# Kernel optimization log

Hardware: AMD Instinct MI355X
Metric: run time of the kernel (lower is better)

## Reference

```python
import jax, jax.numpy as jnp
import numpy as np

N = 512          # nodes per sample (num_nodes)
B = 8            # batch size (samples)
H = 64           # hidden_dim
SPARSITY = 0.1
K = int(SPARSITY * N * (N - 1))  # edges kept per sample (fixed, static)


def setup_inputs() -> dict:
    key = jax.random.key(0)
    ks = jax.random.split(key, 8)

    def lin(k, fi, fo):
        w = jax.random.normal(k, (fi, fo), jnp.float32) / np.sqrt(fi).astype(np.float32)
        b = jnp.zeros((fo,), jnp.float32)
        return w, b

    w_emb, b_emb = lin(ks[0], 1, H)
    w_proj, b_proj = lin(ks[1], H, H)
    w1, b1 = lin(ks[2], 2 * H, H)
    w2, b2 = lin(ks[3], H, H // 2)
    w3, b3 = lin(ks[4], H // 2, 1)
    x = jax.random.uniform(ks[5], (B * N, 1), jnp.float32)  # abundances >= 0
    batch = jnp.repeat(jnp.arange(B, dtype=jnp.int32), N)   # [B*N]
    return dict(x=x, w_emb=w_emb, b_emb=b_emb, w_proj=w_proj, b_proj=b_proj,
                w1=w1, b1=b1, w2=w2, b2=b2, w3=w3, b3=b3, batch=batch)


def reference(x, w_emb, b_emb, w_proj, b_proj, w1, b1, w2, b2, w3, b3, batch):
    # node embedding + projection (dropout is eval-mode no-op)
    emb = jax.nn.relu(x @ w_emb + b_emb) @ w_proj + b_proj     # [B*N, H]
    emb = emb.reshape(B, N, H)
    # first pairwise-MLP layer: cat([e_i, e_j]) @ w1 == e_i @ w1a + e_j @ w1b
    w1a, w1b = w1[:H], w1[H:]
    ai = emb @ w1a                                            # [B, N, H]
    aj = emb @ w1b                                            # [B, N, H]
    h1 = jax.nn.relu(ai[:, :, None, :] + aj[:, None, :, :] + b1)   # [B, N, N, H]
    h2 = jax.nn.relu(jnp.einsum('bijh,hk->bijk', h1, w2) + b2)     # [B, N, N, H/2]
    probs = jax.nn.sigmoid(jnp.einsum('bijk,ko->bij', h2, w3) + b3[0])  # [B, N, N]
    probs = 0.5 * (probs + jnp.swapaxes(probs, 1, 2))          # symmetrize
    probs = probs * (1.0 - jnp.eye(N, dtype=probs.dtype))      # mask diagonal
    flat = probs.reshape(B, N * N)
    _, idx = jax.lax.top_k(flat, K)                            # [B, K]
    idx = jnp.sort(idx, axis=-1)                               # row-major order (dense_to_sparse)
    vals = jnp.take_along_axis(flat, idx, axis=-1)             # [B, K]
    offsets = (jnp.arange(B) * N)[:, None]                     # node offset per sample
    rows = idx // N + offsets
    cols = idx % N + offsets
    edge_index = jnp.stack([rows.reshape(-1), cols.reshape(-1)], axis=0)  # [2, B*K]
    edge_weights = vals.reshape(-1)                            # [B*K]
    adj = jnp.zeros((B, N * N), flat.dtype).at[jnp.arange(B)[:, None], idx].set(vals)
    adj = adj.reshape(B, N, N)                                 # sparse adjacency per sample
    return edge_index, edge_weights, adj
```

## Files before the change

kernel.cpp:

```cpp
#include <hip/hip_runtime.h>

#define NV 512
#define BV 8
#define KSEL 26163
#define NNv (NV*NV)
#define BKv (BV*KSEL)
#define CAPB 32768
#define DELTA 1e-4f

typedef unsigned int u32;
typedef __attribute__((ext_vector_type(2))) float f32x2;
typedef __attribute__((ext_vector_type(4))) float f32x4;
typedef __attribute__((ext_vector_type(4))) u32 u32x4;
typedef __attribute__((ext_vector_type(8))) _Float16 f16x8;

__device__ __forceinline__ f32x2 pk_add(f32x2 a, f32x2 b) {
    f32x2 d; asm("v_pk_add_f32 %0, %1, %2" : "=v"(d) : "v"(a), "v"(b)); return d;
}
__device__ __forceinline__ f32x2 pk_mul(f32x2 a, f32x2 b) {
    f32x2 d; asm("v_pk_mul_f32 %0, %1, %2" : "=v"(d) : "v"(a), "v"(b)); return d;
}
__device__ __forceinline__ f32x2 pk_fma(f32x2 a, f32x2 b, f32x2 c) {
    f32x2 d; asm("v_pk_fma_f32 %0, %1, %2, %3" : "=v"(d) : "v"(a), "v"(b), "v"(c)); return d;
}
__device__ __forceinline__ u32 pkrtz(float a, float b) {
    u32 d; asm("v_cvt_pkrtz_f16_f32 %0, %1, %2" : "=v"(d) : "v"(a), "v"(b)); return d;
}

__global__ void __launch_bounds__(256) k_embed(
    const float* __restrict__ x, const float* __restrict__ w_emb,
    const float* __restrict__ b_emb, const float* __restrict__ w_proj,
    const float* __restrict__ b_proj, const float* __restrict__ w1,
    const float* __restrict__ b1,
    float* __restrict__ ai, float* __restrict__ aj,
    float* __restrict__ ai256, float* __restrict__ ajb256) {
    __shared__ float sh[4][64];
    __shared__ float se[4][64];
    const int c = threadIdx.x;
    const int lr = threadIdx.y;
    const int row = blockIdx.x * 4 + lr;
    const float xv = x[row];
    sh[lr][c] = fmaxf(fmaf(xv, w_emb[c], b_emb[c]), 0.f);
    __syncthreads();
    float e = 0.f;
#pragma unroll
    for (int h = 0; h < 64; ++h) e = fmaf(sh[lr][h], w_proj[h * 64 + c], e);
    se[lr][c] = e + b_proj[c];
    __syncthreads();
    float a0 = 0.f, a1 = 0.f;
#pragma unroll
    for (int h = 0; h < 64; ++h) {
        const float ev = se[lr][h];
        a0 = fmaf(ev, w1[h * 64 + c], a0);
        a1 = fmaf(ev, w1[(64 + h) * 64 + c], a1);
    }
    ai[row * 64 + c] = a0;
    aj[row * 64 + c] = a1;
    ai256[row * 64 + c] = a0 * 256.0f;
    ajb256[row * 64 + c] = (a1 + b1[c]) * 256.0f;
}

__global__ void __launch_bounds__(256) k_pairs_sym(
    const float* __restrict__ ai256, const float* __restrict__ ajb256,
    const float* __restrict__ w2, const float* __restrict__ b2,
    const float* __restrict__ w3, const float* __restrict__ b3,
    float* __restrict__ probs, u32* __restrict__ hist8) {
    __shared__ float sI[2048];
    __shared__ float sJ[2048];
    __shared__ float sp1[32 * 36];
    __shared__ float sp2[32 * 36];
    __shared__ u32 lh[1024];
    const int tid = threadIdx.x;
    const int b = blockIdx.y;
    int remb = blockIdx.x, ta = 0;
    while (remb >= 16 - ta) { remb -= 16 - ta; ++ta; }
    const int tb = ta + remb;
    const int i0 = ta << 5, j0 = tb << 5;
    {
        const int r = tid >> 3, c8 = (tid & 7) << 3;
        const float* srcI = &ai256[(((b << 9) + i0 + r) << 6) + c8];
        *(float4*)&sI[(r << 6) + c8]     = *(const float4*)&srcI[0];
        *(float4*)&sI[(r << 6) + c8 + 4] = *(const float4*)&srcI[4];
        const float* srcJ = &ai256[(((b << 9) + j0 + r) << 6) + c8];
        *(float4*)&sJ[(r << 6) + c8]     = *(const float4*)&srcJ[0];
        *(float4*)&sJ[(r << 6) + c8 + 4] = *(const float4*)&srcJ[4];
        lh[tid] = 0; lh[256 + tid] = 0; lh[512 + tid] = 0; lh[768 + tid] = 0;
    }
    const int lane = tid & 63;
    const int lp = lane & 15, lg = lane >> 4;
    const int wave = tid >> 6;
    const int dir = wave >> 1, wc = wave & 1;
    const int colb = (wc << 4) + lp;
    const int colg = (dir ? i0 : j0) + colb;

    alignas(16) float ajr[2][8];
    {
        const float* base = &ajb256[(((b << 9) + colg) << 6) + (lg << 3)];
        *(float4*)&ajr[0][0] = *(const float4*)&base[0];
        *(float4*)&ajr[0][4] = *(const float4*)&base[4];
        *(float4*)&ajr[1][0] = *(const float4*)&base[32];
        *(float4*)&ajr[1][4] = *(const float4*)&base[36];
    }
    f16x8 Ah[2][2], Al[2][2];
#pragma unroll
    for (int kt = 0; kt < 2; ++kt)
#pragma unroll
        for (int ch = 0; ch < 2; ++ch)
#pragma unroll
            for (int e = 0; e < 8; ++e) {
                const float wv2 = w2[((ch << 5) + (lg << 3) + e) * 32 + (kt << 4) + lp];
                const _Float16 wh = (_Float16)wv2;
                Ah[kt][ch][e] = wh;
                Al[kt][ch][e] = (_Float16)((wv2 - (float)wh) * 2048.0f);
            }
    float b2f[2][4], w3f[2][4];
#pragma unroll
    for (int kt = 0; kt < 2; ++kt)
#pragma unroll
        for (int r = 0; r < 4; ++r) {
            b2f[kt][r] = b2[(kt << 4) + (lg << 2) + r] * 256.0f;
            w3f[kt][r] = w3[(kt << 4) + (lg << 2) + r] * 0.00390625f;
        }
    const float b3v = b3[0];
    __syncthreads();

    const float* __restrict__ sA = dir ? sJ : sI;
    float* __restrict__ spO = dir ? sp2 : sp1;
    const f32x2 C2048 = {2048.f, 2048.f};
    const f32x2 CN2048 = {-2048.f, -2048.f};

    for (int r = 0; r < 32; ++r) {
        alignas(16) float ar[2][8];
        *(float4*)&ar[0][0] = *(const float4*)&sA[(r << 6) + (lg << 3)];
        *(float4*)&ar[0][4] = *(const float4*)&sA[(r << 6) + (lg << 3) + 4];
        *(float4*)&ar[1][0] = *(const float4*)&sA[(r << 6) + 32 + (lg << 3)];
        *(float4*)&ar[1][4] = *(const float4*)&sA[(r << 6) + 32 + (lg << 3) + 4];
        alignas(16) u32 hw[2][4], lw[2][4];
#pragma unroll
        for (int c = 0; c < 2; ++c)
#pragma unroll
            for (int e2 = 0; e2 < 4; ++e2) {
                const f32x2 a2 = *(const f32x2*)&ar[c][e2 * 2];
                const f32x2 j2 = *(const f32x2*)&ajr[c][e2 * 2];
                const f32x2 t2 = pk_add(a2, j2);
                const float u0 = fmaxf(t2[0], 0.f);
                const float u1 = fmaxf(t2[1], 0.f);
                hw[c][e2] = pkrtz(u0, u1);
                f32x2 u2; u2[0] = u0; u2[1] = u1;
                f32x2 hif;
                hif[0] = __uint_as_float(__float_as_uint(u0) & 0xFFFFE000u);
                hif[1] = __uint_as_float(__float_as_uint(u1) & 0xFFFFE000u);
                const f32x2 tm = pk_mul(u2, C2048);
                const f32x2 lo = pk_fma(hif, CN2048, tm);
                lw[c][e2] = pkrtz(lo[0], lo[1]);
            }
        const f16x8 Bh0 = __builtin_bit_cast(f16x8, *(u32x4*)&hw[0][0]);
        const f16x8 Bh1 = __builtin_bit_cast(f16x8, *(u32x4*)&hw[1][0]);
        const f16x8 Bl0 = __builtin_bit_cast(f16x8, *(u32x4*)&lw[0][0]);
        const f16x8 Bl1 = __builtin_bit_cast(f16x8, *(u32x4*)&lw[1][0]);
        f32x4 am0 = {0.f,0.f,0.f,0.f}, am1 = {0.f,0.f,0.f,0.f};
        f32x4 ac0 = {0.f,0.f,0.f,0.f}, ac1 = {0.f,0.f,0.f,0.f};
        am0 = __builtin_amdgcn_mfma_f32_16x16x32_f16(Ah[0][0], Bh0, am0, 0, 0, 0);
        am0 = __builtin_amdgcn_mfma_f32_16x16x32_f16(Ah[0][1], Bh1, am0, 0, 0, 0);
        ac0 = __builtin_amdgcn_mfma_f32_16x16x32_f16(Ah[0][0], Bl0, ac0, 0, 0, 0);
        ac0 = __builtin_amdgcn_mfma_f32_16x16x32_f16(Ah[0][1], Bl1, ac0, 0, 0, 0);
        ac0 = __builtin_amdgcn_mfma_f32_16x16x32_f16(Al[0][0], Bh0, ac0, 0, 0, 0);
        ac0 = __builtin_amdgcn_mfma_f32_16x16x32_f16(Al[0][1], Bh1, ac0, 0, 0, 0);
        am1 = __builtin_amdgcn_mfma_f32_16x16x32_f16(Ah[1][0], Bh0, am1, 0, 0, 0);
        am1 = __builtin_amdgcn_mfma_f32_16x16x32_f16(Ah[1][1], Bh1, am1, 0, 0, 0);
        ac1 = __builtin_amdgcn_mfma_f32_16x16x32_f16(Ah[1][0], Bl0, ac1, 0, 0, 0);
        ac1 = __builtin_amdgcn_mfma_f32_16x16x32_f16(Ah[1][1], Bl1, ac1, 0, 0, 0);
        ac1 = __builtin_amdgcn_mfma_f32_16x16x32_f16(Al[1][0], Bh0, ac1, 0, 0, 0);
        ac1 = __builtin_amdgcn_mfma_f32_16x16x32_f16(Al[1][1], Bh1, ac1, 0, 0, 0);
        float s = 0.f;
#pragma unroll
        for (int q = 0; q < 4; ++q) {
            const float amc = fmaf(ac0[q], 4.8828125e-4f, am0[q]);
            s = fmaf(fmaxf(amc + b2f[0][q], 0.f), w3f[0][q], s);
        }
#pragma unroll
        for (int q = 0; q < 4; ++q) {
            const float amc = fmaf(ac1[q], 4.8828125e-4f, am1[q]);
            s = fmaf(fmaxf(amc + b2f[1][q], 0.f), w3f[1][q], s);
        }
        s += __shfl_xor(s, 16);
        s += __shfl_xor(s, 32);
        const float p = 1.f / (1.f + __expf(-(s + b3v)));
        if (lane < 16) {
            if (dir == 0) spO[r * 36 + colb] = p;
            else          spO[colb * 36 + r] = p;
        }
    }
    __syncthreads();

    {
        const int pr = tid >> 3;
        const int pc = (tid & 7) << 2;
        const int rep = (tid & 3) << 8;
        const bool diag = (ta == tb);
        float4 vo;
        float vq[4];
#pragma unroll
        for (int q = 0; q < 4; ++q) {
            float v = 0.5f * (sp1[pr * 36 + pc + q] + sp2[pr * 36 + pc + q]);
            if (diag && pr == pc + q) v = 0.f;
            vq[q] = v;
            atomicAdd(&lh[rep + (__float_as_uint(v) >> 24)], diag ? 1u : 2u);
        }
        vo.x = vq[0]; vo.y = vq[1]; vo.z = vq[2]; vo.w = vq[3];
        *(float4*)&probs[(((b << 9) + i0 + pr) << 9) + j0 + pc] = vo;
        if (!diag) {
            const int qr = tid >> 3;
            const int qc = (tid & 7) << 2;
            float4 w4;
            w4.x = 0.5f * (sp1[(qc + 0) * 36 + qr] + sp2[(qc + 0) * 36 + qr]);
            w4.y = 0.5f * (sp1[(qc + 1) * 36 + qr] + sp2[(qc + 1) * 36 + qr]);
            w4.z = 0.5f * (sp1[(qc + 2) * 36 + qr] + sp2[(qc + 2) * 36 + qr]);
            w4.w = 0.5f * (sp1[(qc + 3) * 36 + qr] + sp2[(qc + 3) * 36 + qr]);
            *(float4*)&probs[(((b << 9) + j0 + qr) << 9) + i0 + qc] = w4;
        }
    }
    __syncthreads();
    const u32 sum = lh[tid] + lh[256 + tid] + lh[512 + tid] + lh[768 + tid];
    if (sum) atomicAdd(&hist8[b * 256 + tid], sum);
}

__global__ void k_selp8(const u32* __restrict__ hist8, u32* __restrict__ c8,
                        u32* __restrict__ rem1) {
    __shared__ u32 s[256];
    const int b = blockIdx.x, t = threadIdx.x;
    s[t] = hist8[b * 256 + t];
    __syncthreads();
    for (int off = 1; off < 256; off <<= 1) {
        const u32 v = (t + off < 256) ? s[t + off] : 0u;
        __syncthreads();
        s[t] += v;
        __syncthreads();
    }
    const u32 above = (t < 255) ? s[t + 1] : 0u;
    if (s[t] >= (u32)KSEL && above < (u32)KSEL) {
        c8[b] = (u32)t;
        rem1[b] = (u32)KSEL - above;
    }
}

__global__ void __launch_bounds__(256) k_hist13(
    const float* __restrict__ probs, const u32* __restrict__ c8,
    u32* __restrict__ hist13) {
    __shared__ u32 lh[8192];
    const int t = threadIdx.x;
    for (int k = t; k < 8192; k += 256) lh[k] = 0u;
    __syncthreads();
    const int b = blockIdx.y;
    const u32 sel = c8[b];
    const float* Pb = probs + b * NNv;
    const int base = blockIdx.x * 4096 + t;
#pragma unroll
    for (int e = 0; e < 16; ++e) {
        const u32 key = __float_as_uint(Pb[base + e * 256]);
        if ((key >> 24) == sel) atomicAdd(&lh[(key >> 11) & 8191u], 1u);
    }
    __syncthreads();
    for (int k = t; k < 8192; k += 256) {
        const u32 v = lh[k];
        if (v) atomicAdd(&hist13[b * 8192 + k], v);
    }
}

__global__ void k_sel13(const u32* __restrict__ hist13, const u32* __restrict__ c8,
                        const u32* __restrict__ rem1, float* __restrict__ thr) {
    __shared__ u32 s[256];
    const int b = blockIdx.x, t = threadIdx.x;
    const u32* H = hist13 + b * 8192;
    u32 sum = 0;
    for (int k = 0; k < 32; ++k) sum += H[t * 32 + k];
    s[t] = sum;
    __syncthreads();
    for (int off = 1; off < 256; off <<= 1) {
        const u32 v = (t + off < 256) ? s[t + off] : 0u;
        __syncthreads();
        s[t] += v;
        __syncthreads();
    }
    const u32 remv = rem1[b];
    const u32 above = (t < 255) ? s[t + 1] : 0u;
    if (s[t] >= remv && above < remv) {
        u32 cum = above;
        int c = 31;
        for (; c >= 0; --c) {
            cum += H[t * 32 + c];
            if (cum >= remv) break;
        }
        const u32 p21 = (c8[b] << 13) | (u32)(t * 32 + c);
        thr[b]     = __uint_as_float(p21 << 11) - 2.f * DELTA;
        thr[8 + b] = __uint_as_float((p21 + 1u) << 11) + 2.f * DELTA;
    }
}

__global__ void __launch_bounds__(256) k_band(
    const float* __restrict__ P, const float* __restrict__ thr,
    u32* __restrict__ C_in, u32* __restrict__ bandCnt, u32* __restrict__ bandIdx,
    u32* __restrict__ bgt) {
    __shared__ u32 lidx[2048];
    __shared__ u32 lcnt, lhi, gbase;
    const int b = blockIdx.y, blk = blockIdx.x, t = threadIdx.x;
    if (t == 0) { lcnt = 0u; lhi = 0u; }
    __syncthreads();
    const float Tlo = thr[b], Thi = thr[8 + b];
    const int fi0 = blk * 1024 + t * 4;
    const float4 v = *(const float4*)&P[b * NNv + fi0];
    const float vv[4] = {v.x, v.y, v.z, v.w};
    u32 hc = 0;
#pragma unroll
    for (int q = 0; q < 4; ++q) {
        const float xq = vv[q];
        if (xq > Thi) ++hc;
        else if (xq >= Tlo) {
            const u32 p = atomicAdd(&lcnt, 1u);
            if (p < 2048u) lidx[p] = (u32)(fi0 + q);
        }
    }
    if (hc) atomicAdd(&lhi, hc);
    __syncthreads();
    if (t == 0) {
        bgt[b * 256 + blk] = lhi;
        if (lhi) atomicAdd(&C_in[b], lhi);
        gbase = lcnt ? atomicAdd(&bandCnt[b], lcnt) : 0u;
    }
    __syncthreads();
    const u32 ln = min(lcnt, 2048u);
    for (u32 p = t; p < ln; p += 256) {
        const u32 g = gbase + p;
        if (g < (u32)CAPB) bandIdx[b * CAPB + g] = lidx[p];
    }
}

__device__ __forceinline__ float exact_p(const float* __restrict__ rai,
                                         const float* __restrict__ raj,
                                         const float* __restrict__ s_w2,
                                         const float* __restrict__ s_b1,
                                         const float* __restrict__ s_b2,
                                         const float* __restrict__ s_w3,
                                         float b3v) {
    float acc[32];
#pragma unroll
    for (int k = 0; k < 32; ++k) acc[k] = 0.f;
#pragma unroll 1
    for (int h0 = 0; h0 < 64; h0 += 16) {
        float A[16], J[16];
#pragma unroll
        for (int q = 0; q < 4; ++q) {
            *(float4*)&A[q * 4] = *(const float4*)&rai[h0 + q * 4];
            *(float4*)&J[q * 4] = *(const float4*)&raj[h0 + q * 4];
        }
#pragma unroll
        for (int hh = 0; hh < 16; ++hh) {
            const float tv = fmaxf((A[hh] + J[hh]) + s_b1[h0 + hh], 0.f);
#pragma unroll
            for (int k = 0; k < 32; ++k) acc[k] = fmaf(tv, s_w2[(h0 + hh) * 32 + k], acc[k]);
        }
    }
    float d = 0.f;
#pragma unroll
    for (int k = 0; k < 32; ++k) d = fmaf(fmaxf(acc[k] + s_b2[k], 0.f), s_w3[k], d);
    return 1.f / (1.f + expf(-(d + b3v)));
}

__global__ void __launch_bounds__(256) k_band_exact(
    const float* __restrict__ ai, const float* __restrict__ aj,
    const float* __restrict__ b1, const float* __restrict__ w2,
    const float* __restrict__ b2, const float* __restrict__ w3,
    const float* __restrict__ b3, const u32* __restrict__ bandCnt,
    const u32* __restrict__ bandIdx, float* __restrict__ bandVal) {
    __shared__ float s_w2[2048];
    __shared__ float s_b1[64], s_b2[32], s_w3[32];
    const int b = blockIdx.y, t = threadIdx.x;
    {
        const int o = t * 8;
        *(float4*)&s_w2[o]     = *(const float4*)&w2[o];
        *(float4*)&s_w2[o + 4] = *(const float4*)&w2[o + 4];
        if (t < 64) s_b1[t] = b1[t];
        if (t < 32) { s_b2[t] = b2[t]; s_w3[t] = w3[t]; }
    }
    __syncthreads();
    const u32 nb = min(bandCnt[b], (u32)CAPB);
    const float b3v = b3[0];
    for (u32 e = blockIdx.x * 256 + t; e < nb; e += 2048) {
        const u32 idx = bandIdx[b * CAPB + e];
        const int i = (int)(idx >> 9), j = (int)(idx & 511u);
        const float* ri  = &ai[(((b << 9) + i)) << 6];
        const float* rj  = &aj[(((b << 9) + j)) << 6];
        const float* rj2 = &ai[(((b << 9) + j)) << 6];
        const float* ri2 = &aj[(((b << 9) + i)) << 6];
        const float p1 = exact_p(ri, rj, s_w2, s_b1, s_b2, s_w3, b3v);
        const float p2 = exact_p(rj2, ri2, s_w2, s_b1, s_b2, s_w3, b3v);
        bandVal[b * CAPB + e] = 0.5f * (p1 + p2);
    }
}

__global__ void __launch_bounds__(256) k_band_select(
    const u32* __restrict__ bandCnt, const u32* __restrict__ C_in,
    const u32* __restrict__ bandIdx, const float* __restrict__ bandVal,
    u32* __restrict__ bitmap, const u32* __restrict__ bgt,
    u32* __restrict__ goff) {
    __shared__ u32 red[256];
    __shared__ u32 lsel[256];
    __shared__ u32 tie[8192];
    __shared__ u32 tieCnt;
    const int b = blockIdx.x, t = threadIdx.x;
    const u32 nb = min(bandCnt[b], (u32)CAPB);
    const u32 Kp = (u32)KSEL - C_in[b];
    const u32* vb = (const u32*)(bandVal + b * CAPB);
    const u32* ib = bandIdx + b * CAPB;
    u32* bm = bitmap + b * 8192;
    lsel[t] = 0u;
    u32 mn = 0xFFFFFFFFu, mx = 0u;
    for (u32 e = t; e < nb; e += 256) { const u32 v = vb[e]; mn = min(mn, v); mx = max(mx, v); }
    red[t] = mn; __syncthreads();
    for (int s = 128; s > 0; s >>= 1) { if (t < s) red[t] = min(red[t], red[t + s]); __syncthreads(); }
    const u32 glo = red[0]; __syncthreads();
    red[t] = mx; __syncthreads();
    for (int s = 128; s > 0; s >>= 1) { if (t < s) red[t] = max(red[t], red[t + s]); __syncthreads(); }
    const u32 ghi = red[0]; __syncthreads();
    u32 lo = glo, hi = ghi;
    while (lo < hi) {
        const u32 mid = lo + ((hi - lo) >> 1);
        u32 c = 0;
        for (u32 e = t; e < nb; e += 256) c += (vb[e] > mid);
        red[t] = c; __syncthreads();
        for (int s = 128; s > 0; s >>= 1) { if (t < s) red[t] += red[t + s]; __syncthreads(); }
        const u32 tot = red[0]; __syncthreads();
        if (tot >= Kp) lo = mid + 1; else hi = mid;
    }
    const u32 Tx = lo;
    if (t == 0) tieCnt = 0u;
    __syncthreads();
    u32 c = 0;
    for (u32 e = t; e < nb; e += 256) {
        const u32 v = vb[e];
        if (v > Tx) {
            ++c;
            const u32 idx = ib[e];
            atomicOr(&bm[idx >> 5], 1u << (idx & 31u));
            atomicAdd(&lsel[idx >> 10], 1u);
        } else if (v == Tx) {
            const u32 p = atomicAdd(&tieCnt, 1u);
            if (p < 8192u) tie[p] = ib[e];
        }
    }
    red[t] = c; __syncthreads();
    for (int s = 128; s > 0; s >>= 1) { if (t < s) red[t] += red[t + s]; __syncthreads(); }
    const u32 Ap = red[0]; __syncthreads();
    const u32 Rp = Kp - Ap;
    const u32 E = min(tieCnt, 8192u);
    for (u32 e = t; e < E; e += 256) {
        const u32 my = tie[e];
        u32 r = 0;
        for (u32 m = 0; m < E; ++m) r += (tie[m] < my);
        if (r < Rp) {
            atomicOr(&bm[my >> 5], 1u << (my & 31u));
            atomicAdd(&lsel[my >> 10], 1u);
        }
    }
    __syncthreads();
    const u32 g = bgt[b * 256 + t] + lsel[t];
    red[t] = g;
    __syncthreads();
    for (int off = 1; off < 256; off <<= 1) {
        const u32 a = (t >= off) ? red[t - off] : 0u;
        __syncthreads();
        red[t] += a;
        __syncthreads();
    }
    goff[b * 256 + t] = red[t] - g;
}

__global__ void k_write(const float* __restrict__ P, const float* __restrict__ thr,
                        const u32* __restrict__ bitmap, const u32* __restrict__ goff,
                        float* __restrict__ out) {
    __shared__ u32 sg[256];
    const int b = blockIdx.y, blk = blockIdx.x, t = threadIdx.x;
    const float Thi = thr[8 + b];
    const int pbase = b * NNv;
    const int fi0 = blk * 1024 + t * 4;
    const float4 v = *(const float4*)&P[pbase + fi0];
    const float vv[4] = {v.x, v.y, v.z, v.w};
    const u32 w = bitmap[b * 8192 + (fi0 >> 5)];
    const u32 sh = (u32)(fi0 & 31);
    bool sel[4];
    u32 cnt = 0;
#pragma unroll
    for (int q = 0; q < 4; ++q) {
        sel[q] = (vv[q] > Thi) || ((w >> (sh + q)) & 1u);
        cnt += sel[q];
    }
    sg[t] = cnt;
    __syncthreads();
    for (int off = 1; off < 256; off <<= 1) {
        const u32 a = (t >= off) ? sg[t - off] : 0u;
        __syncthreads();
        sg[t] += a;
        __syncthreads();
    }
    u32 pos = goff[b * 256 + blk] + sg[t] - cnt;
#pragma unroll
    for (int q = 0; q < 4; ++q) {
        if (sel[q]) {
            if (pos < (u32)KSEL) {
                const int g = b * KSEL + (int)pos;
                const int fi = fi0 + q;
                const int row = fi >> 9, col = fi & 511;
                out[g]           = (float)(row + (b << 9));
                out[BKv + g]     = (float)(col + (b << 9));
                out[2 * BKv + g] = vv[q];
                out[3 * BKv + pbase + fi] = vv[q];
            }
            ++pos;
        }
    }
}

extern "C" void kernel_launch(void* const* d_in, const int* in_sizes, int n_in,
                              void* d_out, int out_size, void* d_ws, size_t ws_size,
                              hipStream_t stream) {
    const float* x      = (const float*)d_in[0];
    const float* w_emb  = (const float*)d_in[1];
    const float* b_emb  = (const float*)d_in[2];
    const float* w_proj = (const float*)d_in[3];
    const float* b_proj = (const float*)d_in[4];
    const float* w1     = (const float*)d_in[5];
    const float* b1     = (const float*)d_in[6];
    const float* w2     = (const float*)d_in[7];
    const float* b2     = (const float*)d_in[8];
    const float* w3     = (const float*)d_in[9];
    const float* b3     = (const float*)d_in[10];
    (void)in_sizes; (void)n_in; (void)ws_size;

    char* ws = (char*)d_ws;
    float* ai      = (float*)(ws);
    float* aj      = (float*)(ws + 1048576);
    float* ai256   = (float*)(ws + 2097152);
    float* ajb256  = (float*)(ws + 3145728);
    float* probs   = (float*)(ws + 4194304);
    u32*   bandIdx = (u32*)  (ws + 12582912);
    float* bandVal = (float*)(ws + 13631488);
    const size_t SOFF = 14680064;
    u32*   hist8   = (u32*)  (ws + SOFF);
    u32*   hist13  = (u32*)  (ws + SOFF + 8192);
    u32*   c8      = (u32*)  (ws + SOFF + 270336);
    u32*   rem1    = (u32*)  (ws + SOFF + 270368);
    float* thr     = (float*)(ws + SOFF + 270400);
    u32*   C_in    = (u32*)  (ws + SOFF + 270464);
    u32*   bandCnt = (u32*)  (ws + SOFF + 270496);
    u32*   bitmap  = (u32*)  (ws + SOFF + 270528);
    u32*   bgt     = (u32*)  (ws + SOFF + 532672);
    u32*   goff    = (u32*)  (ws + SOFF + 540864);

    float* out = (float*)d_out;

    hipMemsetAsync(d_out, 0, (size_t)out_size * sizeof(float), stream);
    hipMemsetAsync(ws + SOFF, 0, 532672, stream);

    k_embed<<<1024, dim3(64, 4, 1), 0, stream>>>(x, w_emb, b_emb, w_proj, b_proj,
                                                 w1, b1, ai, aj, ai256, ajb256);
    k_pairs_sym<<<dim3(136, 8), 256, 0, stream>>>(ai256, ajb256, w2, b2, w3, b3,
                                                  probs, hist8);
    k_selp8<<<8, 256, 0, stream>>>(hist8, c8, rem1);
    k_hist13<<<dim3(64, 8), 256, 0, stream>>>(probs, c8, hist13);
    k_sel13<<<8, 256, 0, stream>>>(hist13, c8, rem1, thr);
    k_band<<<dim3(256, 8), 256, 0, stream>>>(probs, thr, C_in, bandCnt, bandIdx, bgt);
    k_band_exact<<<dim3(8, 8), 256, 0, stream>>>(ai, aj, b1, w2, b2, w3, b3,
                                                 bandCnt, bandIdx, bandVal);
    k_band_select<<<8, 256, 0, stream>>>(bandCnt, C_in, bandIdx, bandVal,
                                         bitmap, bgt, goff);
    k_write<<<dim3(256, 8), 256, 0, stream>>>(probs, thr, bitmap, goff, out);
}
```

Measured before the change: 206.7 us.

## Fuse selection kernels into producers via last-block-done pattern and trim MFMA work

Each small per-batch selection kernel (selp8, sel13, band_select) is folded into the tail of its producer kernel. The last block to finish, found through an atomic done-counter, runs the prefix scan or selection, which removes three kernel launches and their serialization gaps. k_band_exact moves from 8 grid-stride blocks per batch to 128 one-element-per-thread blocks for more parallelism. It also drops the 2048 scaling in the hi/lo fp16 split so the hi*lo-correction MFMAs accumulate straight into the main accumulator, pads the shared transpose buffer with stride 33 instead of 36, and computes the sigmoid with raw v_exp/v_rcp. The risks are changed rounding in the lo-term split, which may now fall into fp16 subnormals, and the cost of threadfences and atomics.

```diff
diff --git a/kernel.cpp b/kernel.cpp
--- a/kernel.cpp
+++ b/kernel.cpp
@@ -17,14 +17,17 @@
 __device__ __forceinline__ f32x2 pk_add(f32x2 a, f32x2 b) {
     f32x2 d; asm("v_pk_add_f32 %0, %1, %2" : "=v"(d) : "v"(a), "v"(b)); return d;
 }
-__device__ __forceinline__ f32x2 pk_mul(f32x2 a, f32x2 b) {
-    f32x2 d; asm("v_pk_mul_f32 %0, %1, %2" : "=v"(d) : "v"(a), "v"(b)); return d;
-}
 __device__ __forceinline__ f32x2 pk_fma(f32x2 a, f32x2 b, f32x2 c) {
     f32x2 d; asm("v_pk_fma_f32 %0, %1, %2, %3" : "=v"(d) : "v"(a), "v"(b), "v"(c)); return d;
 }
 __device__ __forceinline__ u32 pkrtz(float a, float b) {
     u32 d; asm("v_cvt_pkrtz_f16_f32 %0, %1, %2" : "=v"(d) : "v"(a), "v"(b)); return d;
+}
+__device__ __forceinline__ float fast_sigmoid(float z) {
+    float e, p;
+    asm("v_exp_f32 %0, %1" : "=v"(e) : "v"(-z * 1.44269504f));
+    asm("v_rcp_f32 %0, %1" : "=v"(p) : "v"(1.f + e));
+    return p;
 }
 
 __global__ void __launch_bounds__(256) k_embed(
@@ -64,12 +67,14 @@
     const float* __restrict__ ai256, const float* __restrict__ ajb256,
     const float* __restrict__ w2, const float* __restrict__ b2,
     const float* __restrict__ w3, const float* __restrict__ b3,
-    float* __restrict__ probs, u32* __restrict__ hist8) {
+    float* __restrict__ probs, u32* __restrict__ hist8,
+    u32* __restrict__ done1, u32* __restrict__ c8, u32* __restrict__ rem1) {
     __shared__ float sI[2048];
     __shared__ float sJ[2048];
-    __shared__ float sp1[32 * 36];
-    __shared__ float sp2[32 * 36];
+    __shared__ float sp1[32 * 33];
+    __shared__ float sp2[32 * 33];
     __shared__ u32 lh[1024];
+    __shared__ u32 amLast;
     const int tid = threadIdx.x;
     const int b = blockIdx.y;
     int remb = blockIdx.x, ta = 0;
@@ -77,13 +82,13 @@
     const int tb = ta + remb;
     const int i0 = ta << 5, j0 = tb << 5;
     {
-        const int r = tid >> 3, c8 = (tid & 7) << 3;
-        const float* srcI = &ai256[(((b << 9) + i0 + r) << 6) + c8];
-        *(float4*)&sI[(r << 6) + c8]     = *(const float4*)&srcI[0];
-        *(float4*)&sI[(r << 6) + c8 + 4] = *(const float4*)&srcI[4];
-        const float* srcJ = &ai256[(((b << 9) + j0 + r) << 6) + c8];
-        *(float4*)&sJ[(r << 6) + c8]     = *(const float4*)&srcJ[0];
-        *(float4*)&sJ[(r << 6) + c8 + 4] = *(const float4*)&srcJ[4];
+        const int r = tid >> 3, c8v = (tid & 7) << 3;
+        const float* srcI = &ai256[(((b << 9) + i0 + r) << 6) + c8v];
+        *(float4*)&sI[(r << 6) + c8v]     = *(const float4*)&srcI[0];
+        *(float4*)&sI[(r << 6) + c8v + 4] = *(const float4*)&srcI[4];
+        const float* srcJ = &ai256[(((b << 9) + j0 + r) << 6) + c8v];
+        *(float4*)&sJ[(r << 6) + c8v]     = *(const float4*)&srcJ[0];
+        *(float4*)&sJ[(r << 6) + c8v + 4] = *(const float4*)&srcJ[4];
         lh[tid] = 0; lh[256 + tid] = 0; lh[512 + tid] = 0; lh[768 + tid] = 0;
     }
     const int lane = tid & 63;
@@ -126,8 +131,7 @@
 
     const float* __restrict__ sA = dir ? sJ : sI;
     float* __restrict__ spO = dir ? sp2 : sp1;
-    const f32x2 C2048 = {2048.f, 2048.f};
-    const f32x2 CN2048 = {-2048.f, -2048.f};
+    const f32x2 CN1 = {-1.f, -1.f};
 
     for (int r = 0; r < 32; ++r) {
         alignas(16) float ar[2][8];
@@ -142,16 +146,14 @@
             for (int e2 = 0; e2 < 4; ++e2) {
                 const f32x2 a2 = *(const f32x2*)&ar[c][e2 * 2];
                 const f32x2 j2 = *(const f32x2*)&ajr[c][e2 * 2];
-                const f32x2 t2 = pk_add(a2, j2);
-                const float u0 = fmaxf(t2[0], 0.f);
-                const float u1 = fmaxf(t2[1], 0.f);
-                hw[c][e2] = pkrtz(u0, u1);
-                f32x2 u2; u2[0] = u0; u2[1] = u1;
+                f32x2 u2 = pk_add(a2, j2);
+                u2[0] = fmaxf(u2[0], 0.f);
+                u2[1] = fmaxf(u2[1], 0.f);
+                hw[c][e2] = pkrtz(u2[0], u2[1]);
                 f32x2 hif;
-                hif[0] = __uint_as_float(__float_as_uint(u0) & 0xFFFFE000u);
-                hif[1] = __uint_as_float(__float_as_uint(u1) & 0xFFFFE000u);
-                const f32x2 tm = pk_mul(u2, C2048);
-                const f32x2 lo = pk_fma(hif, CN2048, tm);
+                hif[0] = __uint_as_float(__float_as_uint(u2[0]) & 0xFFFFE000u);
+                hif[1] = __uint_as_float(__float_as_uint(u2[1]) & 0xFFFFE000u);
+                const f32x2 lo = pk_fma(hif, CN1, u2);
                 lw[c][e2] = pkrtz(lo[0], lo[1]);
             }
         const f16x8 Bh0 = __builtin_bit_cast(f16x8, *(u32x4*)&hw[0][0]);
@@ -162,14 +164,14 @@
         f32x4 ac0 = {0.f,0.f,0.f,0.f}, ac1 = {0.f,0.f,0.f,0.f};
         am0 = __builtin_amdgcn_mfma_f32_16x16x32_f16(Ah[0][0], Bh0, am0, 0, 0, 0);
         am0 = __builtin_amdgcn_mfma_f32_16x16x32_f16(Ah[0][1], Bh1, am0, 0, 0, 0);
-        ac0 = __builtin_amdgcn_mfma_f32_16x16x32_f16(Ah[0][0], Bl0, ac0, 0, 0, 0);
-        ac0 = __builtin_amdgcn_mfma_f32_16x16x32_f16(Ah[0][1], Bl1, ac0, 0, 0, 0);
+        am0 = __builtin_amdgcn_mfma_f32_16x16x32_f16(Ah[0][0], Bl0, am0, 0, 0, 0);
+        am0 = __builtin_amdgcn_mfma_f32_16x16x32_f16(Ah[0][1], Bl1, am0, 0, 0, 0);
         ac0 = __builtin_amdgcn_mfma_f32_16x16x32_f16(Al[0][0], Bh0, ac0, 0, 0, 0);
         ac0 = __builtin_amdgcn_mfma_f32_16x16x32_f16(Al[0][1], Bh1, ac0, 0, 0, 0);
         am1 = __builtin_amdgcn_mfma_f32_16x16x32_f16(Ah[1][0], Bh0, am1, 0, 0, 0);
         am1 = __builtin_amdgcn_mfma_f32_16x16x32_f16(Ah[1][1], Bh1, am1, 0, 0, 0);
-        ac1 = __builtin_amdgcn_mfma_f32_16x16x32_f16(Ah[1][0], Bl0, ac1, 0, 0, 0);
-        ac1 = __builtin_amdgcn_mfma_f32_16x16x32_f16(Ah[1][1], Bl1, ac1, 0, 0, 0);
+        am1 = __builtin_amdgcn_mfma_f32_16x16x32_f16(Ah[1][0], Bl0, am1, 0, 0, 0);
+        am1 = __builtin_amdgcn_mfma_f32_16x16x32_f16(Ah[1][1], Bl1, am1, 0, 0, 0);
         ac1 = __builtin_amdgcn_mfma_f32_16x16x32_f16(Al[1][0], Bh0, ac1, 0, 0, 0);
         ac1 = __builtin_amdgcn_mfma_f32_16x16x32_f16(Al[1][1], Bh1, ac1, 0, 0, 0);
         float s = 0.f;
@@ -185,10 +187,10 @@
         }
         s += __shfl_xor(s, 16);
         s += __shfl_xor(s, 32);
-        const float p = 1.f / (1.f + __expf(-(s + b3v)));
+        const float p = fast_sigmoid(s + b3v);
         if (lane < 16) {
-            if (dir == 0) spO[r * 36 + colb] = p;
-            else          spO[colb * 36 + r] = p;
+            if (dir == 0) spO[r * 33 + colb] = p;
+            else          spO[colb * 33 + r] = p;
         }
     }
     __syncthreads();
@@ -202,7 +204,7 @@
         float vq[4];
 #pragma unroll
         for (int q = 0; q < 4; ++q) {
-            float v = 0.5f * (sp1[pr * 36 + pc + q] + sp2[pr * 36 + pc + q]);
+            float v = 0.5f * (sp1[pr * 33 + pc + q] + sp2[pr * 33 + pc + q]);
             if (diag && pr == pc + q) v = 0.f;
             vq[q] = v;
             atomicAdd(&lh[rep + (__float_as_uint(v) >> 24)], diag ? 1u : 2u);
@@ -210,44 +212,46 @@
         vo.x = vq[0]; vo.y = vq[1]; vo.z = vq[2]; vo.w = vq[3];
         *(float4*)&probs[(((b << 9) + i0 + pr) << 9) + j0 + pc] = vo;
         if (!diag) {
-            const int qr = tid >> 3;
-            const int qc = (tid & 7) << 2;
             float4 w4;
-            w4.x = 0.5f * (sp1[(qc + 0) * 36 + qr] + sp2[(qc + 0) * 36 + qr]);
-            w4.y = 0.5f * (sp1[(qc + 1) * 36 + qr] + sp2[(qc + 1) * 36 + qr]);
-            w4.z = 0.5f * (sp1[(qc + 2) * 36 + qr] + sp2[(qc + 2) * 36 + qr]);
-            w4.w = 0.5f * (sp1[(qc + 3) * 36 + qr] + sp2[(qc + 3) * 36 + qr]);
-            *(float4*)&probs[(((b << 9) + j0 + qr) << 9) + i0 + qc] = w4;
+            w4.x = 0.5f * (sp1[(pc + 0) * 33 + pr] + sp2[(pc + 0) * 33 + pr]);
+            w4.y = 0.5f * (sp1[(pc + 1) * 33 + pr] + sp2[(pc + 1) * 33 + pr]);
+            w4.z = 0.5f * (sp1[(pc + 2) * 33 + pr] + sp2[(pc + 2) * 33 + pr]);
+            w4.w = 0.5f * (sp1[(pc + 3) * 33 + pr] + sp2[(pc + 3) * 33 + pr]);
+            *(float4*)&probs[(((b << 9) + j0 + pr) << 9) + i0 + pc] = w4;
         }
     }
     __syncthreads();
     const u32 sum = lh[tid] + lh[256 + tid] + lh[512 + tid] + lh[768 + tid];
     if (sum) atomicAdd(&hist8[b * 256 + tid], sum);
-}
-
-__global__ void k_selp8(const u32* __restrict__ hist8, u32* __restrict__ c8,
-                        u32* __restrict__ rem1) {
-    __shared__ u32 s[256];
-    const int b = blockIdx.x, t = threadIdx.x;
-    s[t] = hist8[b * 256 + t];
+
+    __threadfence();
+    __syncthreads();
+    if (tid == 0) amLast = (atomicAdd(&done1[b], 1u) == 135u) ? 1u : 0u;
+    __syncthreads();
+    if (!amLast) return;
+    __threadfence();
+    u32* s = lh;
+    s[tid] = hist8[b * 256 + tid];
     __syncthreads();
     for (int off = 1; off < 256; off <<= 1) {
-        const u32 v = (t + off < 256) ? s[t + off] : 0u;
-        __syncthreads();
-        s[t] += v;
-        __syncthreads();
-    }
-    const u32 above = (t < 255) ? s[t + 1] : 0u;
-    if (s[t] >= (u32)KSEL && above < (u32)KSEL) {
-        c8[b] = (u32)t;
+        const u32 v = (tid + off < 256) ? s[tid + off] : 0u;
+        __syncthreads();
+        s[tid] += v;
+        __syncthreads();
+    }
+    const u32 above = (tid < 255) ? s[tid + 1] : 0u;
+    if (s[tid] >= (u32)KSEL && above < (u32)KSEL) {
+        c8[b] = (u32)tid;
         rem1[b] = (u32)KSEL - above;
     }
 }
 
 __global__ void __launch_bounds__(256) k_hist13(
     const float* __restrict__ probs, const u32* __restrict__ c8,
-    u32* __restrict__ hist13) {
+    u32* __restrict__ hist13, u32* __restrict__ done2,
+    const u32* __restrict__ rem1, float* __restrict__ thr) {
     __shared__ u32 lh[8192];
+    __shared__ u32 amLast;
     const int t = threadIdx.x;
     for (int k = t; k < 8192; k += 256) lh[k] = 0u;
     __syncthreads();
@@ -265,15 +269,16 @@
         const u32 v = lh[k];
         if (v) atomicAdd(&hist13[b * 8192 + k], v);
     }
-}
-
-__global__ void k_sel13(const u32* __restrict__ hist13, const u32* __restrict__ c8,
-                        const u32* __restrict__ rem1, float* __restrict__ thr) {
-    __shared__ u32 s[256];
-    const int b = blockIdx.x, t = threadIdx.x;
+    __threadfence();
+    __syncthreads();
+    if (t == 0) amLast = (atomicAdd(&done2[b], 1u) == 63u) ? 1u : 0u;
+    __syncthreads();
+    if (!amLast) return;
+    __threadfence();
     const u32* H = hist13 + b * 8192;
     u32 sum = 0;
     for (int k = 0; k < 32; ++k) sum += H[t * 32 + k];
+    __shared__ u32 s[256];
     s[t] = sum;
     __syncthreads();
     for (int off = 1; off < 256; off <<= 1) {
@@ -371,9 +376,17 @@
     const float* __restrict__ b1, const float* __restrict__ w2,
     const float* __restrict__ b2, const float* __restrict__ w3,
     const float* __restrict__ b3, const u32* __restrict__ bandCnt,
-    const u32* __restrict__ bandIdx, float* __restrict__ bandVal) {
+    const u32* __restrict__ bandIdx, float* __restrict__ bandVal,
+    u32* __restrict__ done3, const u32* __restrict__ C_in,
+    u32* __restrict__ bitmap, const u32* __restrict__ bgt,
+    u32* __restrict__ goff) {
     __shared__ float s_w2[2048];
     __shared__ float s_b1[64], s_b2[32], s_w3[32];
+    __shared__ u32 red[256];
+    __shared__ u32 lsel[256];
+    __shared__ u32 tie[8192];
+    __shared__ u32 tieCnt;
+    __shared__ u32 amLast;
     const int b = blockIdx.y, t = threadIdx.x;
     {
         const int o = t * 8;
@@ -384,10 +397,11 @@
     }
     __syncthreads();
     const u32 nb = min(bandCnt[b], (u32)CAPB);
-    const float b3v = b3[0];
-    for (u32 e = blockIdx.x * 256 + t; e < nb; e += 2048) {
+    const u32 e = blockIdx.x * 256 + t;
+    if (e < nb) {
         const u32 idx = bandIdx[b * CAPB + e];
         const int i = (int)(idx >> 9), j = (int)(idx & 511u);
+        const float b3v = b3[0];
         const float* ri  = &ai[(((b << 9) + i)) << 6];
         const float* rj  = &aj[(((b << 9) + j)) << 6];
         const float* rj2 = &ai[(((b << 9) + j)) << 6];
@@ -396,26 +410,19 @@
         const float p2 = exact_p(rj2, ri2, s_w2, s_b1, s_b2, s_w3, b3v);
         bandVal[b * CAPB + e] = 0.5f * (p1 + p2);
     }
-}
-
-__global__ void __launch_bounds__(256) k_band_select(
-    const u32* __restrict__ bandCnt, const u32* __restrict__ C_in,
-    const u32* __restrict__ bandIdx, const float* __restrict__ bandVal,
-    u32* __restrict__ bitmap, const u32* __restrict__ bgt,
-    u32* __restrict__ goff) {
-    __shared__ u32 red[256];
-    __shared__ u32 lsel[256];
-    __shared__ u32 tie[8192];
-    __shared__ u32 tieCnt;
-    const int b = blockIdx.x, t = threadIdx.x;
-    const u32 nb = min(bandCnt[b], (u32)CAPB);
+    __threadfence();
+    __syncthreads();
+    if (t == 0) amLast = (atomicAdd(&done3[b], 1u) == 127u) ? 1u : 0u;
+    __syncthreads();
+    if (!amLast) return;
+    __threadfence();
     const u32 Kp = (u32)KSEL - C_in[b];
     const u32* vb = (const u32*)(bandVal + b * CAPB);
     const u32* ib = bandIdx + b * CAPB;
     u32* bm = bitmap + b * 8192;
     lsel[t] = 0u;
     u32 mn = 0xFFFFFFFFu, mx = 0u;
-    for (u32 e = t; e < nb; e += 256) { const u32 v = vb[e]; mn = min(mn, v); mx = max(mx, v); }
+    for (u32 k = t; k < nb; k += 256) { const u32 v = vb[k]; mn = min(mn, v); mx = max(mx, v); }
     red[t] = mn; __syncthreads();
     for (int s = 128; s > 0; s >>= 1) { if (t < s) red[t] = min(red[t], red[t + s]); __syncthreads(); }
     const u32 glo = red[0]; __syncthreads();
@@ -426,7 +433,7 @@
     while (lo < hi) {
         const u32 mid = lo + ((hi - lo) >> 1);
         u32 c = 0;
-        for (u32 e = t; e < nb; e += 256) c += (vb[e] > mid);
+        for (u32 k = t; k < nb; k += 256) c += (vb[k] > mid);
         red[t] = c; __syncthreads();
         for (int s = 128; s > 0; s >>= 1) { if (t < s) red[t] += red[t + s]; __syncthreads(); }
         const u32 tot = red[0]; __syncthreads();
@@ -436,16 +443,16 @@
     if (t == 0) tieCnt = 0u;
     __syncthreads();
     u32 c = 0;
-    for (u32 e = t; e < nb; e += 256) {
-        const u32 v = vb[e];
+    for (u32 k = t; k < nb; k += 256) {
+        const u32 v = vb[k];
         if (v > Tx) {
             ++c;
-            const u32 idx = ib[e];
+            const u32 idx = ib[k];
             atomicOr(&bm[idx >> 5], 1u << (idx & 31u));
             atomicAdd(&lsel[idx >> 10], 1u);
         } else if (v == Tx) {
             const u32 p = atomicAdd(&tieCnt, 1u);
-            if (p < 8192u) tie[p] = ib[e];
+            if (p < 8192u) tie[p] = ib[k];
         }
     }
     red[t] = c; __syncthreads();
@@ -453,8 +460,8 @@
     const u32 Ap = red[0]; __syncthreads();
     const u32 Rp = Kp - Ap;
     const u32 E = min(tieCnt, 8192u);
-    for (u32 e = t; e < E; e += 256) {
-        const u32 my = tie[e];
+    for (u32 k = t; k < E; k += 256) {
+        const u32 my = tie[k];
         u32 r = 0;
         for (u32 m = 0; m < E; ++m) r += (tie[m] < my);
         if (r < Rp) {
@@ -552,26 +559,26 @@
     float* thr     = (float*)(ws + SOFF + 270400);
     u32*   C_in    = (u32*)  (ws + SOFF + 270464);
     u32*   bandCnt = (u32*)  (ws + SOFF + 270496);
-    u32*   bitmap  = (u32*)  (ws + SOFF + 270528);
-    u32*   bgt     = (u32*)  (ws + SOFF + 532672);
-    u32*   goff    = (u32*)  (ws + SOFF + 540864);
+    u32*   done1   = (u32*)  (ws + SOFF + 270528);
+    u32*   done2   = (u32*)  (ws + SOFF + 270560);
+    u32*   done3   = (u32*)  (ws + SOFF + 270592);
+    u32*   bitmap  = (u32*)  (ws + SOFF + 270624);
+    u32*   bgt     = (u32*)  (ws + SOFF + 532768);
+    u32*   goff    = (u32*)  (ws + SOFF + 540960);
 
     float* out = (float*)d_out;
 
     hipMemsetAsync(d_out, 0, (size_t)out_size * sizeof(float), stream);
-    hipMemsetAsync(ws + SOFF, 0, 532672, stream);
+    hipMemsetAsync(ws + SOFF, 0, 532768, stream);
 
     k_embed<<<1024, dim3(64, 4, 1), 0, stream>>>(x, w_emb, b_emb, w_proj, b_proj,
                                                  w1, b1, ai, aj, ai256, ajb256);
     k_pairs_sym<<<dim3(136, 8), 256, 0, stream>>>(ai256, ajb256, w2, b2, w3, b3,
-                                                  probs, hist8);
-    k_selp8<<<8, 256, 0, stream>>>(hist8, c8, rem1);
-    k_hist13<<<dim3(64, 8), 256, 0, stream>>>(probs, c8, hist13);
-    k_sel13<<<8, 256, 0, stream>>>(hist13, c8, rem1, thr);
+                                                  probs, hist8, done1, c8, rem1);
+    k_hist13<<<dim3(64, 8), 256, 0, stream>>>(probs, c8, hist13, done2, rem1, thr);
     k_band<<<dim3(256, 8), 256, 0, stream>>>(probs, thr, C_in, bandCnt, bandIdx, bgt);
-    k_band_exact<<<dim3(8, 8), 256, 0, stream>>>(ai, aj, b1, w2, b2, w3, b3,
-                                                 bandCnt, bandIdx, bandVal);
-    k_band_select<<<8, 256, 0, stream>>>(bandCnt, C_in, bandIdx, bandVal,
-                                         bitmap, bgt, goff);
+    k_band_exact<<<dim3(128, 8), 256, 0, stream>>>(ai, aj, b1, w2, b2, w3, b3,
+                                                   bandCnt, bandIdx, bandVal,
+                                                   done3, C_in, bitmap, bgt, goff);
     k_write<<<dim3(256, 8), 256, 0, stream>>>(probs, thr, bitmap, goff, out);
 }
```

After: 368.9 us. 78.5% more time.
